# Optimization experiments

Measured on AMD Instinct MI355X. Metric: run time of the kernel, lower is better.

## Reference

```python
import math
import jax, jax.numpy as jnp
import numpy as np

K_KDE = 50
K_RIPS = 16
SCALE = 30.0
DESTNUM = 10
THRESHOLD = 1.0  # hardcoded in topograd_loss
N, D = 8192, 64


def _knn(x, k):
    """Brute-force k-NN with squared L2 distances (faiss IndexFlatL2 semantics,
    self included as nearest neighbour). Returns (sq_dists[N,k], idxs[N,k]),
    neighbours sorted by increasing distance."""
    sq = jnp.sum(x * x, axis=1)
    d = sq[:, None] + sq[None, :] - 2.0 * (x @ x.T)  # [N,N]
    neg, idx = jax.lax.top_k(-d, k)
    return -neg, idx


def _cluster(density, rips_idxs, threshold):
    """Union-find re-implementation of the numba `cluster` routine.
    Iterates points from high density (index N-1) to low; each point joins the
    entry of its highest-index upward neighbour; other upward neighbours'
    entries are merged if their persistence is below threshold, and every
    cross-entry comparison emits a persistence pair (entry_idx, ref_idx).
    Returns the raw pers_pairs array (without the [-1,-1] sentinel rows)."""
    n = density.shape[0]
    parent = np.arange(n)
    name = np.arange(n)  # name[root] = entry id (a point index)

    def find(i):
        root = i
        while parent[root] != root:
            root = parent[root]
        while parent[i] != root:  # path compression
            parent[i], i = root, parent[i]
        return root

    pairs = []
    for i in range(n - 2, -1, -1):
        nbr = rips_idxs[i]
        us = nbr[nbr > i]  # upward (denser, already-processed) neighbours
        if us.size == 0:
            continue  # point i forms its own singleton entry
        e_up = name[find(int(us.max()))]
        parent[find(i)] = find(e_up)  # append i to entry e_up
        for j in us:
            ei = name[find(int(j))]
            if ei != e_up:
                pairs.append((ei, i))
                if density[ei] - density[i] < threshold:
                    parent[find(ei)] = find(e_up)  # merge entry ei into e_up
    return np.asarray(pairs, dtype=np.int64).reshape(-1, 2)


def _pd_pairs(pairs, n):
    """For each unique entry id in pairs[:,0], keep (entry_id, max ref idx)."""
    maxref = np.full(n, -1, dtype=np.int64)
    np.maximum.at(maxref, pairs[:, 0], pairs[:, 1])
    uniq = np.unique(pairs[:, 0])
    return np.stack([uniq, maxref[uniq]], axis=1)


def setup_inputs() -> dict:
    key = jax.random.key(0)
    x = jax.random.normal(key, (N, D), dtype=jnp.float32)
    return {"x": x}


def reference(x):
    # --- KNN kernel density estimate (differentiable) ---
    vals, _ = _knn(x, K_KDE)
    res = jnp.sum(jnp.exp(-vals / SCALE), axis=1) / (K_KDE * SCALE)
    dens = res / jnp.max(res)
    # --- sort by ascending density ---
    sorted_idxs = jnp.argsort(dens)
    dens_s = dens[sorted_idxs]
    x_s = x[sorted_idxs]
    # --- delta-Rips graph on sorted points ---
    _, rips_idxs = _knn(x_s, K_RIPS)
    # --- persistence clustering (non-differentiable, host) ---
    pairs = _cluster(np.asarray(dens_s), np.asarray(rips_idxs), THRESHOLD)
    pd = jnp.asarray(_pd_pairs(pairs, x.shape[0]))  # [P,2] int64
    # --- topological loss ---
    oripd = dens_s[pd]  # [P,2] (birth, death) densities
    sidx = jnp.argsort(oripd[:, 0] - oripd[:, 1])  # ascending persistence
    changepairs = pd[sidx[:-DESTNUM]]
    nochangepairs = pd[sidx[-DESTNUM:-1]]
    dest = jax.lax.stop_gradient(oripd[sidx[-1]])  # torch.as_tensor detaches
    pd11 = dens_s[changepairs]
    weakdist = jnp.sum(pd11[:, 0] - pd11[:, 1]) / math.sqrt(2.0)
    strongdist = jnp.sum(jnp.linalg.norm(dens_s[nochangepairs] - dest, axis=1))
    return weakdist + strongdist
```

## Files before the change

### kernel.cpp

```cpp
#include <hip/hip_runtime.h>
#include <stdint.h>

#define NN 8192
#define DD 64

using bf16x8 = __attribute__((ext_vector_type(8))) short;
using f32x4  = __attribute__((ext_vector_type(4))) float;

__device__ __forceinline__ unsigned short f2bf(float f){
  unsigned u = __float_as_uint(f);
  return (unsigned short)((u + 0x7FFFu + ((u >> 16) & 1u)) >> 16);
}

__global__ __launch_bounds__(256) void k_pre(const float* __restrict__ x, float* __restrict__ xT,
                                             float* __restrict__ sq, int do_tr,
                                             uint4* __restrict__ xfrag, int do_frag){
  __shared__ float tile[64*65];
  const int tid = threadIdx.x;
  const int b = blockIdx.x;
  for (int k = 0; k < 4; ++k){
    const int idx4 = tid + k*256;
    const float4 v = ((const float4*)(x + (size_t)b*4096))[idx4];
    const int row = idx4 >> 4, d0 = (idx4 & 15) * 4;
    tile[row*65 + d0 + 0] = v.x;
    tile[row*65 + d0 + 1] = v.y;
    tile[row*65 + d0 + 2] = v.z;
    tile[row*65 + d0 + 3] = v.w;
  }
  __syncthreads();
  if (do_tr){
    const int jj = tid & 15;
    const int dq = tid >> 4;
    for (int k = 0; k < 4; ++k){
      const int d = dq + 16*k;
      float4 o;
      o.x = tile[(jj*4+0)*65 + d];
      o.y = tile[(jj*4+1)*65 + d];
      o.z = tile[(jj*4+2)*65 + d];
      o.w = tile[(jj*4+3)*65 + d];
      ((float4*)xT)[(size_t)d*2048 + b*16 + jj] = o;
    }
  }
  if (do_frag){
    for (int ch = tid; ch < 512; ch += 256){
      const int c  = ch & 15;
      const int q  = (ch >> 4) & 3;
      const int m  = (ch >> 6) & 1;
      const int gl = ch >> 7;
      const float* sp = tile + (gl*16 + c)*65 + m*32 + q*8;
      unsigned short h[8];
#pragma unroll
      for (int i2 = 0; i2 < 8; ++i2) h[i2] = f2bf(sp[i2]);
      uint4 o;
      o.x = (unsigned)h[0] | ((unsigned)h[1] << 16);
      o.y = (unsigned)h[2] | ((unsigned)h[3] << 16);
      o.z = (unsigned)h[4] | ((unsigned)h[5] << 16);
      o.w = (unsigned)h[6] | ((unsigned)h[7] << 16);
      xfrag[(size_t)b*512 + ch] = o;
    }
  }
  if (tid < 64){
    float acc = 0.f;
    const float* rp = tile + tid*65;
    for (int d = 0; d < 64; ++d) acc = fmaf(rp[d], rp[d], acc);
    sq[b*64 + tid] = acc;
  }
}

template<bool XT>
__device__ __forceinline__ void dists_1024(const float* __restrict__ x, const float* __restrict__ xT,
                                           const float* __restrict__ xi, int jbase, int tid,
                                           float acc[8][4]){
#pragma unroll
  for (int r = 0; r < 8; ++r)
#pragma unroll
    for (int q = 0; q < 4; ++q) acc[r][q] = 0.f;
  const int j0 = jbase + tid*4;
  for (int dq = 0; dq < 16; ++dq){
    float4 vj[4];
    if (XT){
#pragma unroll
      for (int s = 0; s < 4; ++s)
        vj[s] = ((const float4*)xT)[(size_t)(dq*4+s)*2048 + (j0 >> 2)];
    } else {
#pragma unroll
      for (int s = 0; s < 4; ++s){
        const int d = dq*4 + s;
        vj[s].x = x[(size_t)(j0+0)*64 + d];
        vj[s].y = x[(size_t)(j0+1)*64 + d];
        vj[s].z = x[(size_t)(j0+2)*64 + d];
        vj[s].w = x[(size_t)(j0+3)*64 + d];
      }
    }
#pragma unroll
    for (int r = 0; r < 8; ++r){
      const float4 wv = ((const float4*)(xi + r*64))[dq];
      acc[r][0] = fmaf(vj[0].x, wv.x, acc[r][0]);
      acc[r][1] = fmaf(vj[0].y, wv.x, acc[r][1]);
      acc[r][2] = fmaf(vj[0].z, wv.x, acc[r][2]);
      acc[r][3] = fmaf(vj[0].w, wv.x, acc[r][3]);
      acc[r][0] = fmaf(vj[1].x, wv.y, acc[r][0]);
      acc[r][1] = fmaf(vj[1].y, wv.y, acc[r][1]);
      acc[r][2] = fmaf(vj[1].z, wv.y, acc[r][2]);
      acc[r][3] = fmaf(vj[1].w, wv.y, acc[r][3]);
      acc[r][0] = fmaf(vj[2].x, wv.z, acc[r][0]);
      acc[r][1] = fmaf(vj[2].y, wv.z, acc[r][1]);
      acc[r][2] = fmaf(vj[2].z, wv.z, acc[r][2]);
      acc[r][3] = fmaf(vj[2].w, wv.z, acc[r][3]);
      acc[r][0] = fmaf(vj[3].x, wv.w, acc[r][0]);
      acc[r][1] = fmaf(vj[3].y, wv.w, acc[r][1]);
      acc[r][2] = fmaf(vj[3].z, wv.w, acc[r][2]);
      acc[r][3] = fmaf(vj[3].w, wv.w, acc[r][3]);
    }
  }
}

template<bool XT, bool MF>
__global__ __launch_bounds__(256) void k_cand(const float* __restrict__ x, const float* __restrict__ xT,
                                              const float* __restrict__ sq,
                                              float* __restrict__ res, unsigned short* __restrict__ nn16,
                                              const uint4* __restrict__ xfrag){
  __shared__ __align__(16) float xi[8*64];
  __shared__ float sqi_s[16];
  __shared__ float tubs[16];
  __shared__ __align__(16) unsigned long long cand[8*512];
  __shared__ unsigned ccnt[8];
  __shared__ unsigned ccnt2[8];
  __shared__ unsigned short candidx[MF ? 8*1024 : 16];
  float* samp = (float*)cand;
  const int tid = threadIdx.x;
  const int i0 = blockIdx.x * 8;
  for (int t = tid; t < 8*64; t += 256) xi[t] = x[(size_t)i0*64 + t];
  if (tid < 16){
    sqi_s[tid] = (tid < 8) ? sq[i0+tid] : 0.f;
    tubs[tid] = 0.f;
    if (tid < 8){ ccnt[tid] = 0u; ccnt2[tid] = 0u; }
  }
  __syncthreads();
  float sqir[8];
#pragma unroll
  for (int r = 0; r < 8; ++r) sqir[r] = sqi_s[r];

  const int w0 = (blockIdx.x * 1024) & 8191;
  {
    float acc[8][4];
    dists_1024<XT>(x, xT, xi, w0, tid, acc);
    float sqj[4];
#pragma unroll
    for (int q = 0; q < 4; ++q) sqj[q] = sq[w0 + tid*4 + q];
#pragma unroll
    for (int r = 0; r < 8; ++r)
#pragma unroll
      for (int q = 0; q < 4; ++q)
        samp[r*1024 + tid*4 + q] = (sqir[r] + sqj[q]) - 2.f*acc[r][q];
  }
  __syncthreads();
  {
    const int wv = tid >> 6, lane = tid & 63;
    for (int rr = 0; rr < 2; ++rr){
      const int r = wv + rr*4;
      float v[16];
#pragma unroll
      for (int k2 = 0; k2 < 16; ++k2) v[k2] = samp[r*1024 + lane + 64*k2];
      unsigned lo = 0u, hi = 0x7F800001u;
      while (hi - lo > 1u){
        const unsigned mid = (lo + hi) >> 1;
        const float pf = __uint_as_float(mid);
        int c = 0;
#pragma unroll
        for (int k2 = 0; k2 < 16; ++k2) c += (v[k2] < pf) ? 1 : 0;
#pragma unroll
        for (int off = 32; off; off >>= 1) c += __shfl_xor(c, off);
        if (c >= 32) hi = mid; else lo = mid;
      }
      if (lane == 0) tubs[r] = __uint_as_float(hi);
    }
  }
  __syncthreads();
  float tubr[8];
#pragma unroll
  for (int r = 0; r < 8; ++r) tubr[r] = tubs[r];
  for (int t = tid; t < 8*512; t += 256) cand[t] = ~0ULL;
  __syncthreads();

  if constexpr (MF){
    const int l   = tid & 63;
    const int w   = tid >> 6;
    const int qh  = l >> 4;
    const int c16 = l & 15;
    bf16x8 a0, a1;
#pragma unroll
    for (int i2 = 0; i2 < 8; ++i2){ a0[i2] = 0; a1[i2] = 0; }
    if (c16 < 8){
      const float* ap = xi + c16*64 + qh*8;
#pragma unroll
      for (int i2 = 0; i2 < 8; ++i2){
        a0[i2] = (short)f2bf(ap[i2]);
        a1[i2] = (short)f2bf(ap[i2 + 32]);
      }
    }
    float thr2v[4];
#pragma unroll
    for (int rg = 0; rg < 4; ++rg) thr2v[rg] = tubs[qh*4 + rg] + 2.0f - sqi_s[qh*4 + rg];

    const bf16x8* bfp = (const bf16x8*)xfrag + (size_t)w*128 + l;
    const float*  sqp = sq + w*16 + c16;
    for (int it = 0; it < 128; ++it){
      const bf16x8 b0 = bfp[(size_t)it*512];
      const bf16x8 b1 = bfp[(size_t)it*512 + 64];
      f32x4 acc = {0.f, 0.f, 0.f, 0.f};
      acc = __builtin_amdgcn_mfma_f32_16x16x32_bf16(a0, b0, acc, 0, 0, 0);
      acc = __builtin_amdgcn_mfma_f32_16x16x32_bf16(a1, b1, acc, 0, 0, 0);
      const float sqj = sqp[it*64];
      if (l < 32){
        const int j = (it*4 + w)*16 + c16;
#pragma unroll
        for (int rg = 0; rg < 4; ++rg){
          const float v = fmaf(-2.f, acc[rg], sqj);
          if (v < thr2v[rg]){
            const int r = qh*4 + rg;
            const unsigned pos = atomicAdd(&ccnt2[r], 1u);
            if (pos < 1024u) candidx[r*1024 + pos] = (unsigned short)j;
          }
        }
      }
    }
    __syncthreads();
    for (int r = 0; r < 8; ++r){
      const int cnt = ((int)ccnt2[r] < 1024) ? (int)ccnt2[r] : 1024;
      for (int t = tid; t < cnt; t += 256){
        const int j = candidx[r*1024 + t];
        const float* xj = x + (size_t)j*64;
        const float* xr = xi + r*64;
        float acc = 0.f;
#pragma unroll
        for (int d4 = 0; d4 < 16; ++d4){
          const float4 vj4 = ((const float4*)xj)[d4];
          const float4 wi4 = ((const float4*)xr)[d4];
          acc = fmaf(vj4.x, wi4.x, acc);
          acc = fmaf(vj4.y, wi4.y, acc);
          acc = fmaf(vj4.z, wi4.z, acc);
          acc = fmaf(vj4.w, wi4.w, acc);
        }
        const float dist = (sqir[r] + sq[j]) - 2.f*acc;
        if (dist < tubs[r]){
          const unsigned pos = atomicAdd(&ccnt[r], 1u);
          if (pos < 512u){
            unsigned u = __float_as_uint(dist);
            u = ((int)u < 0) ? ~u : (u | 0x80000000u);
            cand[r*512 + pos] = (((unsigned long long)u) << 13) | (unsigned)j;
          }
        }
      }
    }
  } else {
    for (int pass = 0; pass < 8; ++pass){
      const int jb = pass*1024;
      float acc[8][4];
      dists_1024<XT>(x, xT, xi, jb, tid, acc);
      const int j0 = jb + tid*4;
      float sqj[4];
#pragma unroll
      for (int q = 0; q < 4; ++q) sqj[q] = sq[j0 + q];
#pragma unroll
      for (int r = 0; r < 8; ++r){
#pragma unroll
        for (int q = 0; q < 4; ++q){
          const float dist = (sqir[r] + sqj[q]) - 2.f*acc[r][q];
          if (dist < tubr[r]){
            const unsigned pos = atomicAdd(&ccnt[r], 1u);
            if (pos < 512u){
              unsigned u = __float_as_uint(dist);
              u = ((int)u < 0) ? ~u : (u | 0x80000000u);
              cand[r*512 + pos] = (((unsigned long long)u) << 13) | (unsigned)(j0 + q);
            }
          }
        }
      }
    }
  }
  __syncthreads();

  for (int k = 2; k <= 512; k <<= 1){
    for (int jj2 = k >> 1; jj2 > 0; jj2 >>= 1){
      const int mm = tid;
      const int i = ((mm & ~(jj2-1)) << 1) | (mm & (jj2-1));
      const int p = i | jj2;
      const bool up2 = ((i & k) == 0);
#pragma unroll
      for (int r = 0; r < 8; ++r){
        unsigned long long a = cand[r*512+i], bb = cand[r*512+p];
        if ((a > bb) == up2){ cand[r*512+i] = bb; cand[r*512+p] = a; }
      }
      __syncthreads();
    }
  }

  const int wv2 = tid >> 6, lane2 = tid & 63;
  for (int rr = 0; rr < 2; ++rr){
    const int r = wv2*2 + rr;
    const unsigned long long kk = cand[r*512 + lane2];
    float e = 0.f;
    if (lane2 < 50){
      unsigned u2 = (unsigned)(kk >> 13);
      u2 = (u2 & 0x80000000u) ? (u2 & 0x7FFFFFFFu) : ~u2;
      e = expf(-__uint_as_float(u2) / 30.f);
    }
#pragma unroll
    for (int off = 32; off; off >>= 1) e += __shfl_down(e, off);
    if (lane2 == 0) res[i0+r] = e / 1500.f;
    if (lane2 < 16) nn16[(size_t)(i0+r)*16 + lane2] = (unsigned short)(kk & 8191ULL);
  }
}

__device__ __forceinline__ unsigned long long shfl64_xor(unsigned long long v, int off){
  return (((unsigned long long)(unsigned)__shfl_xor((int)(v >> 32), off)) << 32)
       | (unsigned long long)(unsigned)__shfl_xor((int)(v & 0xFFFFFFFFu), off);
}

__global__ __launch_bounds__(256) void k_rank(const float* __restrict__ res,
                                              unsigned short* __restrict__ rank,
                                              float* __restrict__ dens_s){
  __shared__ __align__(16) unsigned long long keys[NN];
  __shared__ float red[256];
  __shared__ unsigned short pcnt[256];
  const int tid = threadIdx.x;
  float m = 0.f;
  for (int t = tid; t < NN; t += 256) m = fmaxf(m, res[t]);
  red[tid] = m; __syncthreads();
  for (int o = 128; o; o >>= 1){ if (tid < o) red[tid] = fmaxf(red[tid], red[tid+o]); __syncthreads(); }
  const float mr = red[0];
  __syncthreads();
  for (int t = tid; t < NN; t += 256){
    const float dnv = res[t] / mr;
    keys[t] = (((unsigned long long)__float_as_uint(dnv)) << 13) | (unsigned)t;
  }
  __syncthreads();
  const int i = blockIdx.x*128 + (tid & 127);
  const unsigned long long ki = keys[i];
  const int j0 = (tid >> 7) * (NN/2);
  int c = 0;
#pragma unroll 8
  for (int j = 0; j < NN/2; ++j) c += (keys[j0 + j] < ki) ? 1 : 0;
  pcnt[tid] = (unsigned short)c;
  __syncthreads();
  if (tid < 128){
    const int r = (int)pcnt[tid] + (int)pcnt[tid + 128];
    rank[i] = (unsigned short)r;
    dens_s[r] = __uint_as_float((unsigned)(ki >> 13));
  }
}

__global__ __launch_bounds__(256) void k_ups(const unsigned short* __restrict__ rank,
                                             const unsigned short* __restrict__ nn16,
                                             unsigned short* __restrict__ ups_t){
  __shared__ __align__(16) unsigned short rk[NN];
  const int tid = threadIdx.x;
  for (int t = tid; t < NN/8; t += 256) ((uint4*)rk)[t] = ((const uint4*)rank)[t];
  __syncthreads();
  const int o = blockIdx.x*256 + tid;
  const int p = rk[o];
  const uint4 n0 = ((const uint4*)nn16)[(size_t)o*2];
  const uint4 n1 = ((const uint4*)nn16)[(size_t)o*2 + 1];
  unsigned nw[8] = {n0.x, n0.y, n0.z, n0.w, n1.x, n1.y, n1.z, n1.w};
  unsigned short outv[16];
  int cnt = 0;
  for (int k = 0; k < 16; ++k){
    const unsigned nb = (nw[k >> 1] >> ((k & 1) * 16)) & 0xFFFFu;
    const unsigned r = rk[nb];
    if ((int)r > p){
      int q = cnt++;
      while (q > 0 && outv[q-1] < (unsigned short)r){ outv[q] = outv[q-1]; --q; }
      outv[q] = (unsigned short)r;
    }
  }
  for (int k = cnt; k < 16; ++k) outv[k] = 0;
  unsigned short* dst = ups_t + (size_t)p*16;
  uint4 a, b;
  a.x = (unsigned)outv[0] | ((unsigned)outv[1] << 16);
  a.y = (unsigned)outv[2] | ((unsigned)outv[3] << 16);
  a.z = (unsigned)outv[4] | ((unsigned)outv[5] << 16);
  a.w = (unsigned)outv[6] | ((unsigned)outv[7] << 16);
  b.x = (unsigned)outv[8] | ((unsigned)outv[9] << 16);
  b.y = (unsigned)outv[10] | ((unsigned)outv[11] << 16);
  b.z = (unsigned)outv[12] | ((unsigned)outv[13] << 16);
  b.w = (unsigned)outv[14] | ((unsigned)outv[15] << 16);
  ((uint4*)dst)[0] = a;
  ((uint4*)dst)[1] = b;
}

__device__ __forceinline__ unsigned uf_find2(volatile unsigned short* comp, unsigned x){
  unsigned r = comp[x];
  while (true){
    const unsigned g = comp[r];
    if (g == r) break;
    comp[x] = (unsigned short)g;
    x = r; r = g;
  }
  return r;
}

__global__ __launch_bounds__(1024) void k_msf(const float* __restrict__ dens_s,
                                              unsigned short* __restrict__ ups_t,
                                              unsigned long long* __restrict__ edges,
                                              int edgecap,
                                              float* __restrict__ out){
  __shared__ __align__(16) float dens[NN];
  __shared__ __align__(16) unsigned short P[NN];
  __shared__ __align__(16) unsigned short pkid[NN];
  __shared__ __align__(16) unsigned short death[NN];
  __shared__ __align__(16) unsigned short pkrank[4096];
  __shared__ __align__(16) unsigned short comp[4096];
  __shared__ __align__(16) unsigned short hook[4096];
  __shared__ __align__(16) unsigned bestv[4096];
  __shared__ __align__(16) unsigned long long msf[4096];
  __shared__ unsigned long long wred[17];
  __shared__ unsigned long long sel[10];
  __shared__ unsigned ecnt_s, ecnt2_s, mcnt_s, chg_s, flat_s, dcnt_s;
  unsigned* scan1 = (unsigned*)msf;
  float* red = (float*)msf;
  unsigned* dlist = bestv;

  const int tid = threadIdx.x;
  const int lane = tid & 63;

  for (int t = tid; t < NN/4; t += 1024)
    ((float4*)dens)[t] = ((const float4*)dens_s)[t];
  for (int t = tid; t < NN; t += 1024){
    const unsigned u0 = ups_t[(size_t)t*16];
    P[t] = (u0 == 0u) ? (unsigned short)t : (unsigned short)u0;
    death[t] = 0xFFFFu;
  }
  if (tid == 0){ ecnt_s = 0u; mcnt_s = 0u; dcnt_s = 0u; }
  __syncthreads();

  for (int rd = 0; rd < 13; ++rd){
    for (int pp = 0; pp < 8; ++pp){
      const int p = tid + pp*1024;
      const unsigned v = P[p];
      const unsigned w2 = P[v];
      if (w2 != v) P[p] = (unsigned short)w2;
    }
    __syncthreads();
  }

  {
    const int p0 = tid*8;
    int c = 0;
    for (int k = 0; k < 8; ++k) c += (P[p0+k] == (unsigned short)(p0+k)) ? 1 : 0;
    scan1[tid] = (unsigned)c; __syncthreads();
    for (int s = 1; s < 1024; s <<= 1){
      const unsigned v = scan1[tid];
      const unsigned u = (tid >= s) ? scan1[tid-s] : 0u;
      __syncthreads();
      scan1[tid] = v + u;
      __syncthreads();
    }
    int base = (int)scan1[tid] - c;
    for (int k = 0; k < 8; ++k){
      const int p = p0 + k;
      if (P[p] == (unsigned short)p){
        pkid[p] = (unsigned short)base;
        if (base < 4096) pkrank[base] = (unsigned short)p;
        ++base;
      }
    }
  }
  __syncthreads();
  int Npk = (int)scan1[1023];
  if (Npk > 4096) Npk = 4096;
  __syncthreads();

  for (int pp = 0; pp < 8; ++pp){
    const int p = tid + pp*1024;
    const uint4 a4 = ((const uint4*)ups_t)[(size_t)p*2];
    const uint4 b4 = ((const uint4*)ups_t)[(size_t)p*2 + 1];
    unsigned uu[8] = {a4.x, a4.y, a4.z, a4.w, b4.x, b4.y, b4.z, b4.w};
    unsigned edv[15];
    int nd = 0;
    const unsigned u0 = uu[0] & 0xFFFFu;
    if (u0 != 0u){
      const unsigned m0 = P[u0];
      const unsigned m0id = pkid[m0];
      for (int k = 1; k < 16; ++k){
        const unsigned uk = (uu[k >> 1] >> ((k & 1) * 16)) & 0xFFFFu;
        if (uk == 0u) break;
        const unsigned v = P[uk];
        if (v == m0) continue;
        const unsigned vid = pkid[v];
        bool dup = false;
        for (int j = 0; j < nd; ++j) dup = dup || ((edv[j] >> 16) == vid);
        if (dup) continue;
        edv[nd++] = (vid << 16) | m0id;
      }
    }
    unsigned off = (unsigned)nd;
    for (int s = 1; s < 64; s <<= 1){
      const unsigned o = (unsigned)__shfl_up((int)off, s);
      if (lane >= s) off += o;
    }
    const unsigned tot = (unsigned)__shfl((int)off, 63);
    unsigned wb = 0u;
    if (lane == 0 && tot) wb = atomicAdd(&ecnt_s, tot);
    wb = (unsigned)__shfl((int)wb, 0);
    const unsigned mybase = wb + off - (unsigned)nd;
    for (int k = 0; k < nd; ++k){
      const unsigned pos = mybase + (unsigned)k;
      if ((int)pos < edgecap)
        edges[pos] = (((unsigned long long)(unsigned)p) << 32) | (unsigned long long)edv[k];
    }
  }
  __syncthreads();
  int Ecur = ((int)ecnt_s < edgecap) ? (int)ecnt_s : edgecap;

  unsigned long long* eb_in  = edges;
  unsigned long long* eb_out = (unsigned long long*)ups_t;
  for (int t = tid; t < Npk; t += 1024) comp[t] = (unsigned short)t;
  __syncthreads();
  for (int round = 0; round < 16 && Ecur > 0; ++round){
    for (int t = tid; t < Npk; t += 1024){ bestv[t] = 0u; hook[t] = 0xFFFFu; }
    if (tid == 0){ chg_s = 0u; ecnt2_s = 0u; }
    __syncthreads();
    for (int base = 0; base < Ecur; base += 1024){
      const int e = base + tid;
      bool keep = false;
      unsigned long long ed = 0ULL;
      if (e < Ecur){
        ed = eb_in[e];
        const unsigned a = (unsigned)(ed >> 16) & 0xFFFFu;
        const unsigned b = (unsigned)ed & 0xFFFFu;
        const unsigned ra = comp[a], rb = comp[b];
        if (ra != rb){
          keep = true;
          const unsigned key = ((((unsigned)(ed >> 32)) + 1u) << 18) | (unsigned)e;
          atomicMax(&bestv[ra], key);
          atomicMax(&bestv[rb], key);
        }
      }
      const unsigned long long bal = __ballot(keep);
      const unsigned cnt = (unsigned)__popcll(bal);
      const unsigned pfx = (unsigned)__popcll(bal & ((1ULL << lane) - 1ULL));
      unsigned wb = 0u;
      if (lane == 0 && cnt) wb = atomicAdd(&ecnt2_s, cnt);
      wb = (unsigned)__shfl((int)wb, 0);
      if (keep && (wb + pfx) < 32768u) eb_out[wb + pfx] = ed;
    }
    __syncthreads();
    for (int t = tid; t < Npk; t += 1024){
      if (comp[t] == (unsigned short)t && bestv[t] != 0u){
        const unsigned long long ed = eb_in[bestv[t] & 0x3FFFFu];
        const unsigned a = (unsigned)(ed >> 16) & 0xFFFFu;
        const unsigned b = (unsigned)ed & 0xFFFFu;
        const unsigned ra = comp[a], rb = comp[b];
        hook[t] = (unsigned short)((ra == (unsigned)t) ? rb : ra);
      }
    }
    __syncthreads();
    for (int t = tid; t < Npk; t += 1024){
      const unsigned o = hook[t];
      if (o != 0xFFFFu && !(hook[o] == (unsigned short)t && (unsigned)t < o)){
        comp[t] = (unsigned short)o;
        chg_s = 1u;
        const unsigned long long ed = eb_in[bestv[t] & 0x3FFFFu];
        const unsigned pos = atomicAdd(&mcnt_s, 1u);
        if (pos < 4096u) msf[pos] = (((ed >> 32) + 1ULL) << 32) | (ed & 0xFFFFFFFFULL);
      }
    }
    __syncthreads();
    for (;;){
      if (tid == 0) flat_s = 0u;
      __syncthreads();
      for (int t = tid; t < Npk; t += 1024){
        const unsigned c = comp[t];
        const unsigned cc = comp[c];
        if (cc != c){ comp[t] = (unsigned short)cc; flat_s = 1u; }
      }
      __syncthreads();
      if (flat_s == 0u) break;
    }
    const int En = ((int)ecnt2_s < 32768) ? (int)ecnt2_s : 32767;
    const unsigned ch = chg_s;
    __syncthreads();
    Ecur = En;
    { unsigned long long* t2 = eb_in; eb_in = eb_out; eb_out = t2; }
    if (ch == 0u) break;
  }

  const int M = ((int)mcnt_s < 4096) ? (int)mcnt_s : 4095;
  int W = 64; while (W < M) W <<= 1;
  for (int t = M + tid; t < W; t += 1024) msf[t] = 0ULL;
  for (int t = tid; t < Npk; t += 1024) comp[t] = (unsigned short)t;
  __syncthreads();
  for (int k = 2; k <= W; k <<= 1){
    for (int j = k >> 1; j > 0; j >>= 1){
      for (int m2 = tid; m2 < W/2; m2 += 1024){
        const int i = ((m2 & ~(j-1)) << 1) | (m2 & (j-1));
        const int p = i | j;
        const bool up = ((i & k) == 0);
        const unsigned long long a = msf[i], b = msf[p];
        if ((a < b) == up){ msf[i] = b; msf[p] = a; }
      }
      __syncthreads();
    }
  }

  {
    const int nb = (M + 63) >> 6;
    for (int bch = 0; bch < nb; ++bch){
      if (tid < 64){
        const int ei = bch*64 + lane;
        unsigned ra = 0xFFFFu, rb = 0xFFFFu, wgt = 0u;
        if (ei < M){
          const unsigned long long e = msf[ei];
          const unsigned a = ((unsigned)e >> 16) & 0xFFFFu;
          const unsigned b = (unsigned)e & 0xFFFFu;
          wgt = (unsigned)(e >> 32) - 1u;
          ra = uf_find2(comp, a);
          rb = uf_find2(comp, b);
        }
        unsigned kra = 0xFFFFu, krb = 0xFFFFu;
        for (int i = 0; i < 64; ++i){
          const unsigned rai = (unsigned)__builtin_amdgcn_readlane((int)ra, i);
          const unsigned rbi = (unsigned)__builtin_amdgcn_readlane((int)rb, i);
          if (rai == 0xFFFFu || rai == rbi) continue;
          if (lane == i){ kra = rai; krb = rbi; }
          ra = (ra == rai) ? rbi : ra;
          rb = (rb == rai) ? rbi : rb;
        }
        if (kra != 0xFFFFu){
          death[pkrank[kra]] = (unsigned short)wgt;
          comp[kra] = (unsigned short)krb;
        }
      }
      __syncthreads();
      for (int t = tid; t < Npk; t += 1024){
        const unsigned c = comp[t];
        const unsigned cc = comp[c];
        if (cc != c) comp[t] = (unsigned short)cc;
      }
      __syncthreads();
    }
  }
  __syncthreads();

  float s = 0.f;
  for (int e = tid; e < NN; e += 1024){
    const int dr = death[e];
    if (dr != 0xFFFF) s += dens[e] - dens[dr];
  }
  red[tid] = s; __syncthreads();
  for (int o = 512; o; o >>= 1){ if (tid < o) red[tid] += red[tid+o]; __syncthreads(); }
  const float S = red[0];

  for (int e8 = 0; e8 < 8; ++e8){
    const int e = tid + e8*1024;
    const int dr = death[e];
    const bool have = (dr != 0xFFFF);
    const unsigned long long bal = __ballot(have);
    const unsigned cnt = (unsigned)__popcll(bal);
    const unsigned pfx = (unsigned)__popcll(bal & ((1ULL << lane) - 1ULL));
    unsigned wb = 0u;
    if (lane == 0 && cnt) wb = atomicAdd(&dcnt_s, cnt);
    wb = (unsigned)__shfl((int)wb, 0);
    if (have && (wb + pfx) < 4096u) dlist[wb + pfx] = ((unsigned)e << 13) | (unsigned)dr;
  }
  __syncthreads();
  const int Dm = ((int)dcnt_s < 4096) ? (int)dcnt_s : 4096;

  unsigned long long last = ~0ULL;
  for (int t10 = 0; t10 < 10; ++t10){
    unsigned long long km = 0ULL;
    for (int i = tid; i < Dm; i += 1024){
      const unsigned pk = dlist[i];
      const unsigned e = pk >> 13, dr = pk & 8191u;
      const float pers = dens[e] - dens[dr];
      const unsigned long long k = (((unsigned long long)__float_as_uint(pers)) << 13) | e;
      if (k < last && k > km) km = k;
    }
    for (int off = 32; off; off >>= 1){
      const unsigned long long o = shfl64_xor(km, off);
      km = (o > km) ? o : km;
    }
    if (lane == 0) wred[tid >> 6] = km;
    __syncthreads();
    if (tid < 64){
      unsigned long long v = (tid < 16) ? wred[tid] : 0ULL;
      for (int off = 8; off; off >>= 1){
        const unsigned long long o = shfl64_xor(v, off);
        v = (o > v) ? o : v;
      }
      if (tid == 0) wred[16] = v;
    }
    __syncthreads();
    const unsigned long long st = wred[16];
    if (tid == 0) sel[t10] = st;
    last = st;
    __syncthreads();
  }
  if (tid == 0){
    float top = 0.f;
    for (int t10 = 0; t10 < 10; ++t10)
      if (sel[t10]) top += __uint_as_float((unsigned)(sel[t10] >> 13));
    float strong = 0.f, dest0 = 0.f, dest1 = 0.f;
    if (sel[0]){
      const unsigned e0 = (unsigned)(sel[0] & 8191ULL);
      dest0 = dens[e0]; dest1 = dens[death[e0]];
    }
    for (int t10 = 1; t10 < 10; ++t10){
      if (!sel[t10]) continue;
      const unsigned e = (unsigned)(sel[t10] & 8191ULL);
      const float a = dens[e] - dest0;
      const float b = dens[death[e]] - dest1;
      strong += sqrtf(a*a + b*b);
    }
    out[0] = (S - top) / 1.41421356237309515f + strong;
  }
}

extern "C" void kernel_launch(void* const* d_in, const int* in_sizes, int n_in,
                              void* d_out, int out_size, void* d_ws, size_t ws_size,
                              hipStream_t stream){
  const float* x = (const float*)d_in[0];
  char* w = (char*)d_ws;
  float*          sq     = (float*)(w + 0);
  float*          res    = (float*)(w + 32768);
  float*          dens_s = (float*)(w + 65536);
  unsigned short* rank   = (unsigned short*)(w + 98304);
  unsigned short* nn16   = (unsigned short*)(w + 114688);
  unsigned short* ups_t  = (unsigned short*)(w + 376832);
  float*          xT     = (float*)(w + 655360);
  uint4*          xfrag  = (uint4*)(w + 655360 + (size_t)NN*DD*4);
  const int use_xt = (ws_size >= (size_t)(655360 + NN*DD*4)) ? 1 : 0;
  const int use_mf = (ws_size >= (size_t)(655360 + NN*DD*4 + NN*DD*2)) ? 1 : 0;
  unsigned long long* edges = use_xt ? (unsigned long long*)(w + 655360)
                                     : (unsigned long long*)(w + 114688);
  const int edgecap = use_xt ? 262143 : 32767;

  k_pre<<<128, 256, 0, stream>>>(x, xT, sq, use_xt, xfrag, use_mf);
  if (use_mf)      k_cand<true , true ><<<1024, 256, 0, stream>>>(x, xT, sq, res, nn16, xfrag);
  else if (use_xt) k_cand<true , false><<<1024, 256, 0, stream>>>(x, xT, sq, res, nn16, xfrag);
  else             k_cand<false, false><<<1024, 256, 0, stream>>>(x, xT, sq, res, nn16, xfrag);
  k_rank<<<64, 256, 0, stream>>>(res, rank, dens_s);
  k_ups <<<32, 256, 0, stream>>>(rank, nn16, ups_t);
  k_msf <<<1, 1024, 0, stream>>>(dens_s, ups_t, edges, edgecap, (float*)d_out);
}
```

Measured before the change: 633.3 us.

## Replace atomic candidate lists with ballot bitmasks and prefetch MFMA fragments

In the MFMA filtering pass, threshold hits are no longer appended to a per-row LDS list through shared-memory atomics. Each wave now builds hit bitmasks with __ballot and stores them in LDS, and the exact refinement pass walks those bitmasks with ctz. The B-fragment and squared-norm loads are also software-prefetched four iterations ahead in registers, to hide global latency behind the MFMAs. This removes atomic contention and the 1024-candidate cap. The cost is more register pressure, and the refinement work is spread unevenly across threads, since each one scans a 16-bit mask.

```diff
diff --git a/kernel.cpp b/kernel.cpp
--- a/kernel.cpp
+++ b/kernel.cpp
@@ -125,8 +125,7 @@
   __shared__ float tubs[16];
   __shared__ __align__(16) unsigned long long cand[8*512];
   __shared__ unsigned ccnt[8];
-  __shared__ unsigned ccnt2[8];
-  __shared__ unsigned short candidx[MF ? 8*1024 : 16];
+  __shared__ __align__(16) unsigned bm32s[MF ? 512*4 : 4];
   float* samp = (float*)cand;
   const int tid = threadIdx.x;
   const int i0 = blockIdx.x * 8;
@@ -134,7 +133,7 @@
   if (tid < 16){
     sqi_s[tid] = (tid < 8) ? sq[i0+tid] : 0.f;
     tubs[tid] = 0.f;
-    if (tid < 8){ ccnt[tid] = 0u; ccnt2[tid] = 0u; }
+    if (tid < 8) ccnt[tid] = 0u;
   }
   __syncthreads();
   float sqir[8];
@@ -199,39 +198,65 @@
         a1[i2] = (short)f2bf(ap[i2 + 32]);
       }
     }
-    float thr2v[4];
-#pragma unroll
-    for (int rg = 0; rg < 4; ++rg) thr2v[rg] = tubs[qh*4 + rg] + 2.0f - sqi_s[qh*4 + rg];
+    const float thr2v0 = tubs[qh*4+0] + 2.0f - sqi_s[qh*4+0];
+    const float thr2v1 = tubs[qh*4+1] + 2.0f - sqi_s[qh*4+1];
+    const float thr2v2 = tubs[qh*4+2] + 2.0f - sqi_s[qh*4+2];
+    const float thr2v3 = tubs[qh*4+3] + 2.0f - sqi_s[qh*4+3];
 
     const bf16x8* bfp = (const bf16x8*)xfrag + (size_t)w*128 + l;
     const float*  sqp = sq + w*16 + c16;
-    for (int it = 0; it < 128; ++it){
-      const bf16x8 b0 = bfp[(size_t)it*512];
-      const bf16x8 b1 = bfp[(size_t)it*512 + 64];
+
+    auto fbody = [&](bf16x8 B0v, bf16x8 B1v, float SJ, int ITV){
       f32x4 acc = {0.f, 0.f, 0.f, 0.f};
-      acc = __builtin_amdgcn_mfma_f32_16x16x32_bf16(a0, b0, acc, 0, 0, 0);
-      acc = __builtin_amdgcn_mfma_f32_16x16x32_bf16(a1, b1, acc, 0, 0, 0);
-      const float sqj = sqp[it*64];
-      if (l < 32){
-        const int j = (it*4 + w)*16 + c16;
-#pragma unroll
-        for (int rg = 0; rg < 4; ++rg){
-          const float v = fmaf(-2.f, acc[rg], sqj);
-          if (v < thr2v[rg]){
-            const int r = qh*4 + rg;
-            const unsigned pos = atomicAdd(&ccnt2[r], 1u);
-            if (pos < 1024u) candidx[r*1024 + pos] = (unsigned short)j;
-          }
-        }
-      }
-    }
-    __syncthreads();
-    for (int r = 0; r < 8; ++r){
-      const int cnt = ((int)ccnt2[r] < 1024) ? (int)ccnt2[r] : 1024;
-      for (int t = tid; t < cnt; t += 256){
-        const int j = candidx[r*1024 + t];
+      acc = __builtin_amdgcn_mfma_f32_16x16x32_bf16(a0, B0v, acc, 0, 0, 0);
+      acc = __builtin_amdgcn_mfma_f32_16x16x32_bf16(a1, B1v, acc, 0, 0, 0);
+      const float v0 = fmaf(-2.f, acc[0], SJ);
+      const float v1 = fmaf(-2.f, acc[1], SJ);
+      const float v2 = fmaf(-2.f, acc[2], SJ);
+      const float v3 = fmaf(-2.f, acc[3], SJ);
+      const unsigned long long m0 = __ballot(v0 < thr2v0);
+      const unsigned long long m1 = __ballot(v1 < thr2v1);
+      const unsigned long long m2 = __ballot(v2 < thr2v2);
+      const unsigned long long m3 = __ballot(v3 < thr2v3);
+      const int cc = ITV*4 + w;
+      if (l == 0){
+        bm32s[cc*4+0] = ((unsigned)m0 & 0xFFFFu) | (((unsigned)m1 & 0xFFFFu) << 16);
+        bm32s[cc*4+1] = ((unsigned)m2 & 0xFFFFu) | (((unsigned)m3 & 0xFFFFu) << 16);
+      } else if (l == 16){
+        bm32s[cc*4+2] = (((unsigned)m0 >> 16) & 0xFFFFu) | ((((unsigned)m1 >> 16) & 0xFFFFu) << 16);
+        bm32s[cc*4+3] = (((unsigned)m2 >> 16) & 0xFFFFu) | ((((unsigned)m3 >> 16) & 0xFFFFu) << 16);
+      }
+    };
+
+    bf16x8 pA0 = bfp[0],    pA1 = bfp[64];
+    bf16x8 pB0 = bfp[512],  pB1 = bfp[512+64];
+    bf16x8 pC0 = bfp[1024], pC1 = bfp[1024+64];
+    bf16x8 pD0 = bfp[1536], pD1 = bfp[1536+64];
+    float sA = sqp[0], sB = sqp[64], sC = sqp[128], sD = sqp[192];
+    for (int itb = 0; itb < 128; itb += 4){
+      fbody(pA0, pA1, sA, itb);
+      if (itb + 4 < 128){ pA0 = bfp[(size_t)(itb+4)*512]; pA1 = bfp[(size_t)(itb+4)*512+64]; sA = sqp[(itb+4)*64]; }
+      fbody(pB0, pB1, sB, itb+1);
+      if (itb + 5 < 128){ pB0 = bfp[(size_t)(itb+5)*512]; pB1 = bfp[(size_t)(itb+5)*512+64]; sB = sqp[(itb+5)*64]; }
+      fbody(pC0, pC1, sC, itb+2);
+      if (itb + 6 < 128){ pC0 = bfp[(size_t)(itb+6)*512]; pC1 = bfp[(size_t)(itb+6)*512+64]; sC = sqp[(itb+6)*64]; }
+      fbody(pD0, pD1, sD, itb+3);
+      if (itb + 7 < 128){ pD0 = bfp[(size_t)(itb+7)*512]; pD1 = bfp[(size_t)(itb+7)*512+64]; sD = sqp[(itb+7)*64]; }
+    }
+    __syncthreads();
+
+    const unsigned short* bmu = (const unsigned short*)bm32s;
+    for (int idx = tid; idx < 4096; idx += 256){
+      const int cc = idx >> 3, r = idx & 7;
+      unsigned msk = (unsigned)bmu[cc*8 + r];
+      const float* xr = xi + r*64;
+      const float sqi_r = sqir[r];
+      const float tub_r = tubr[r];
+      while (msk){
+        const int bpos = __builtin_ctz(msk);
+        msk &= msk - 1u;
+        const int j = cc*16 + bpos;
         const float* xj = x + (size_t)j*64;
-        const float* xr = xi + r*64;
         float acc = 0.f;
 #pragma unroll
         for (int d4 = 0; d4 < 16; ++d4){
@@ -242,8 +267,8 @@
           acc = fmaf(vj4.z, wi4.z, acc);
           acc = fmaf(vj4.w, wi4.w, acc);
         }
-        const float dist = (sqir[r] + sq[j]) - 2.f*acc;
-        if (dist < tubs[r]){
+        const float dist = (sqi_r + sq[j]) - 2.f*acc;
+        if (dist < tub_r){
           const unsigned pos = atomicAdd(&ccnt[r], 1u);
           if (pos < 512u){
             unsigned u = __float_as_uint(dist);
```

New measurement: 641.9 us. No clear change (+1.4%).

## Split fused candidate kernel into sample, MFMA filter bitmask, and exact-sort kernels

Applied to the files above, without the earlier changes.

The single k_cand kernel is split into three kernels. k_samp computes the per-row sample threshold. k_filt runs the bf16 MFMA prefilter with software-prefetched fragments and writes a per-pair bitmask to global memory. k_csort decodes the bitmask, recomputes exact distances and bitonic-sorts. The split lowers per-kernel shared-memory and register pressure and removes LDS atomics from the MFMA loop, which should allow higher occupancy. In exchange it adds two extra launches and an 8 MB global bitmask round-trip, and it needs a larger workspace or it falls back to the old path.

```diff
diff --git a/kernel.cpp b/kernel.cpp
--- a/kernel.cpp
+++ b/kernel.cpp
@@ -115,123 +115,155 @@
   }
 }
 
-template<bool XT, bool MF>
-__global__ __launch_bounds__(256) void k_cand(const float* __restrict__ x, const float* __restrict__ xT,
-                                              const float* __restrict__ sq,
-                                              float* __restrict__ res, unsigned short* __restrict__ nn16,
-                                              const uint4* __restrict__ xfrag){
+template<bool XT>
+__global__ __launch_bounds__(256) void k_samp(const float* __restrict__ x, const float* __restrict__ xT,
+                                              const float* __restrict__ sq, float* __restrict__ tub){
   __shared__ __align__(16) float xi[8*64];
-  __shared__ float sqi_s[16];
-  __shared__ float tubs[16];
-  __shared__ __align__(16) unsigned long long cand[8*512];
-  __shared__ unsigned ccnt[8];
-  __shared__ unsigned ccnt2[8];
-  __shared__ unsigned short candidx[MF ? 8*1024 : 16];
-  float* samp = (float*)cand;
+  __shared__ float sqi_s[8];
+  __shared__ __align__(16) float samp[8*1024];
   const int tid = threadIdx.x;
   const int i0 = blockIdx.x * 8;
   for (int t = tid; t < 8*64; t += 256) xi[t] = x[(size_t)i0*64 + t];
-  if (tid < 16){
-    sqi_s[tid] = (tid < 8) ? sq[i0+tid] : 0.f;
-    tubs[tid] = 0.f;
-    if (tid < 8){ ccnt[tid] = 0u; ccnt2[tid] = 0u; }
-  }
+  if (tid < 8) sqi_s[tid] = sq[i0+tid];
   __syncthreads();
   float sqir[8];
 #pragma unroll
   for (int r = 0; r < 8; ++r) sqir[r] = sqi_s[r];
 
   const int w0 = (blockIdx.x * 1024) & 8191;
-  {
-    float acc[8][4];
-    dists_1024<XT>(x, xT, xi, w0, tid, acc);
-    float sqj[4];
-#pragma unroll
-    for (int q = 0; q < 4; ++q) sqj[q] = sq[w0 + tid*4 + q];
-#pragma unroll
-    for (int r = 0; r < 8; ++r)
-#pragma unroll
-      for (int q = 0; q < 4; ++q)
-        samp[r*1024 + tid*4 + q] = (sqir[r] + sqj[q]) - 2.f*acc[r][q];
-  }
-  __syncthreads();
-  {
-    const int wv = tid >> 6, lane = tid & 63;
-    for (int rr = 0; rr < 2; ++rr){
-      const int r = wv + rr*4;
-      float v[16];
-#pragma unroll
-      for (int k2 = 0; k2 < 16; ++k2) v[k2] = samp[r*1024 + lane + 64*k2];
-      unsigned lo = 0u, hi = 0x7F800001u;
-      while (hi - lo > 1u){
-        const unsigned mid = (lo + hi) >> 1;
-        const float pf = __uint_as_float(mid);
-        int c = 0;
-#pragma unroll
-        for (int k2 = 0; k2 < 16; ++k2) c += (v[k2] < pf) ? 1 : 0;
-#pragma unroll
-        for (int off = 32; off; off >>= 1) c += __shfl_xor(c, off);
-        if (c >= 32) hi = mid; else lo = mid;
-      }
-      if (lane == 0) tubs[r] = __uint_as_float(hi);
-    }
-  }
-  __syncthreads();
-  float tubr[8];
-#pragma unroll
-  for (int r = 0; r < 8; ++r) tubr[r] = tubs[r];
+  float acc[8][4];
+  dists_1024<XT>(x, xT, xi, w0, tid, acc);
+  float sqj[4];
+#pragma unroll
+  for (int q = 0; q < 4; ++q) sqj[q] = sq[w0 + tid*4 + q];
+#pragma unroll
+  for (int r = 0; r < 8; ++r)
+#pragma unroll
+    for (int q = 0; q < 4; ++q)
+      samp[r*1024 + tid*4 + q] = (sqir[r] + sqj[q]) - 2.f*acc[r][q];
+  __syncthreads();
+  const int wv = tid >> 6, lane = tid & 63;
+  for (int rr = 0; rr < 2; ++rr){
+    const int r = wv + rr*4;
+    float v[16];
+#pragma unroll
+    for (int k2 = 0; k2 < 16; ++k2) v[k2] = samp[r*1024 + lane + 64*k2];
+    unsigned lo = 0u, hi = 0x7F800001u;
+    while (hi - lo > 1u){
+      const unsigned mid = (lo + hi) >> 1;
+      const float pf = __uint_as_float(mid);
+      int c = 0;
+#pragma unroll
+      for (int k2 = 0; k2 < 16; ++k2) c += (v[k2] < pf) ? 1 : 0;
+#pragma unroll
+      for (int off = 32; off; off >>= 1) c += __shfl_xor(c, off);
+      if (c >= 32) hi = mid; else lo = mid;
+    }
+    if (lane == 0) tub[i0 + r] = __uint_as_float(hi);
+  }
+}
+
+__global__ __launch_bounds__(256) void k_filt(const float* __restrict__ x, const float* __restrict__ sq,
+                                              const float* __restrict__ tub,
+                                              const uint4* __restrict__ xfrag,
+                                              unsigned char* __restrict__ nib){
+  const int tid = threadIdx.x;
+  const int l   = tid & 63;
+  const int w   = tid >> 6;
+  const int qh  = l >> 4;
+  const int c16 = l & 15;
+  const int i0  = blockIdx.x * 8;
+
+  bf16x8 a0, a1;
+#pragma unroll
+  for (int i2 = 0; i2 < 8; ++i2){ a0[i2] = 0; a1[i2] = 0; }
+  if (c16 < 8){
+    const float* ap = x + (size_t)(i0 + c16)*64 + qh*8;
+#pragma unroll
+    for (int i2 = 0; i2 < 8; ++i2){
+      a0[i2] = (short)f2bf(ap[i2]);
+      a1[i2] = (short)f2bf(ap[i2 + 32]);
+    }
+  }
+  float thr2[4];
+#pragma unroll
+  for (int rg = 0; rg < 4; ++rg){
+    int row = qh*4 + rg; row = (row < 8) ? row : 0;
+    thr2[rg] = tub[i0 + row] + 2.0f - sq[i0 + row];
+  }
+
+  const bf16x8* bfp = (const bf16x8*)xfrag + (size_t)w*128 + l;
+  const float*  sqp = sq + w*16 + c16;
+  unsigned char* nb = nib + (size_t)blockIdx.x*8192 + w*16 + c16;
+
+  bf16x8 A0 = bfp[0],   A1 = bfp[64];     float SA = sqp[0];
+  bf16x8 B0 = bfp[512], B1 = bfp[512+64]; float SB = sqp[64];
+  for (int it = 0; it < 128; it += 2){
+    const int n2 = (it+2 < 128) ? it+2 : 126;
+    const int n3 = (it+3 < 128) ? it+3 : 127;
+    bf16x8 N0 = bfp[(size_t)n2*512], N1 = bfp[(size_t)n2*512 + 64];
+    bf16x8 M0 = bfp[(size_t)n3*512], M1 = bfp[(size_t)n3*512 + 64];
+    const float SN = sqp[n2*64], SM = sqp[n3*64];
+    {
+      f32x4 acc = {0.f, 0.f, 0.f, 0.f};
+      acc = __builtin_amdgcn_mfma_f32_16x16x32_bf16(a0, A0, acc, 0, 0, 0);
+      acc = __builtin_amdgcn_mfma_f32_16x16x32_bf16(a1, A1, acc, 0, 0, 0);
+      unsigned m4 = 0u;
+      m4 |= (fmaf(-2.f, acc[0], SA) < thr2[0]) ? 1u : 0u;
+      m4 |= (fmaf(-2.f, acc[1], SA) < thr2[1]) ? 2u : 0u;
+      m4 |= (fmaf(-2.f, acc[2], SA) < thr2[2]) ? 4u : 0u;
+      m4 |= (fmaf(-2.f, acc[3], SA) < thr2[3]) ? 8u : 0u;
+      const unsigned pm = (unsigned)__shfl((int)m4, (l + 16) & 63);
+      if (l < 16) nb[it*64] = (unsigned char)(m4 | (pm << 4));
+    }
+    {
+      f32x4 acc = {0.f, 0.f, 0.f, 0.f};
+      acc = __builtin_amdgcn_mfma_f32_16x16x32_bf16(a0, B0, acc, 0, 0, 0);
+      acc = __builtin_amdgcn_mfma_f32_16x16x32_bf16(a1, B1, acc, 0, 0, 0);
+      unsigned m4 = 0u;
+      m4 |= (fmaf(-2.f, acc[0], SB) < thr2[0]) ? 1u : 0u;
+      m4 |= (fmaf(-2.f, acc[1], SB) < thr2[1]) ? 2u : 0u;
+      m4 |= (fmaf(-2.f, acc[2], SB) < thr2[2]) ? 4u : 0u;
+      m4 |= (fmaf(-2.f, acc[3], SB) < thr2[3]) ? 8u : 0u;
+      const unsigned pm = (unsigned)__shfl((int)m4, (l + 16) & 63);
+      if (l < 16) nb[(it+1)*64] = (unsigned char)(m4 | (pm << 4));
+    }
+    A0 = N0; A1 = N1; SA = SN;
+    B0 = M0; B1 = M1; SB = SM;
+  }
+}
+
+__global__ __launch_bounds__(256) void k_csort(const float* __restrict__ x, const float* __restrict__ sq,
+                                               const float* __restrict__ tub,
+                                               const unsigned char* __restrict__ nib,
+                                               float* __restrict__ res, unsigned short* __restrict__ nn16){
+  __shared__ __align__(16) float xi[8*68];
+  __shared__ float sqi_s[8];
+  __shared__ float tubs[8];
+  __shared__ __align__(16) unsigned long long cand[8*512];
+  __shared__ unsigned ccnt[8];
+  const int tid = threadIdx.x;
+  const int i0 = blockIdx.x * 8;
+  for (int t = tid; t < 8*64; t += 256) xi[(t >> 6)*68 + (t & 63)] = x[(size_t)i0*64 + t];
+  if (tid < 8){ sqi_s[tid] = sq[i0+tid]; tubs[tid] = tub[i0+tid]; ccnt[tid] = 0u; }
   for (int t = tid; t < 8*512; t += 256) cand[t] = ~0ULL;
   __syncthreads();
 
-  if constexpr (MF){
-    const int l   = tid & 63;
-    const int w   = tid >> 6;
-    const int qh  = l >> 4;
-    const int c16 = l & 15;
-    bf16x8 a0, a1;
-#pragma unroll
-    for (int i2 = 0; i2 < 8; ++i2){ a0[i2] = 0; a1[i2] = 0; }
-    if (c16 < 8){
-      const float* ap = xi + c16*64 + qh*8;
-#pragma unroll
-      for (int i2 = 0; i2 < 8; ++i2){
-        a0[i2] = (short)f2bf(ap[i2]);
-        a1[i2] = (short)f2bf(ap[i2 + 32]);
-      }
-    }
-    float thr2v[4];
-#pragma unroll
-    for (int rg = 0; rg < 4; ++rg) thr2v[rg] = tubs[qh*4 + rg] + 2.0f - sqi_s[qh*4 + rg];
-
-    const bf16x8* bfp = (const bf16x8*)xfrag + (size_t)w*128 + l;
-    const float*  sqp = sq + w*16 + c16;
-    for (int it = 0; it < 128; ++it){
-      const bf16x8 b0 = bfp[(size_t)it*512];
-      const bf16x8 b1 = bfp[(size_t)it*512 + 64];
-      f32x4 acc = {0.f, 0.f, 0.f, 0.f};
-      acc = __builtin_amdgcn_mfma_f32_16x16x32_bf16(a0, b0, acc, 0, 0, 0);
-      acc = __builtin_amdgcn_mfma_f32_16x16x32_bf16(a1, b1, acc, 0, 0, 0);
-      const float sqj = sqp[it*64];
-      if (l < 32){
-        const int j = (it*4 + w)*16 + c16;
-#pragma unroll
-        for (int rg = 0; rg < 4; ++rg){
-          const float v = fmaf(-2.f, acc[rg], sqj);
-          if (v < thr2v[rg]){
-            const int r = qh*4 + rg;
-            const unsigned pos = atomicAdd(&ccnt2[r], 1u);
-            if (pos < 1024u) candidx[r*1024 + pos] = (unsigned short)j;
-          }
-        }
-      }
-    }
-    __syncthreads();
-    for (int r = 0; r < 8; ++r){
-      const int cnt = ((int)ccnt2[r] < 1024) ? (int)ccnt2[r] : 1024;
-      for (int t = tid; t < cnt; t += 256){
-        const int j = candidx[r*1024 + t];
+  const uint4* nb4 = (const uint4*)(nib + (size_t)blockIdx.x*8192);
+  for (int u = tid; u < 512; u += 256){
+    const uint4 v4 = nb4[u];
+    unsigned wds[4] = {v4.x, v4.y, v4.z, v4.w};
+#pragma unroll
+    for (int ww = 0; ww < 4; ++ww){
+      unsigned wvv = wds[ww];
+      while (wvv){
+        const int bit = __builtin_ctz(wvv);
+        wvv &= wvv - 1u;
+        const int byte = bit >> 3;
+        const int r = bit & 7;
+        const int j = u*16 + ww*4 + byte;
         const float* xj = x + (size_t)j*64;
-        const float* xr = xi + r*64;
+        const float* xr = xi + r*68;
         float acc = 0.f;
 #pragma unroll
         for (int d4 = 0; d4 < 16; ++d4){
@@ -242,38 +274,132 @@
           acc = fmaf(vj4.z, wi4.z, acc);
           acc = fmaf(vj4.w, wi4.w, acc);
         }
-        const float dist = (sqir[r] + sq[j]) - 2.f*acc;
+        const float dist = (sqi_s[r] + sq[j]) - 2.f*acc;
         if (dist < tubs[r]){
+          const unsigned pos = atomicAdd(&ccnt[r], 1u);
+          if (pos < 512u){
+            unsigned u2 = __float_as_uint(dist);
+            u2 = ((int)u2 < 0) ? ~u2 : (u2 | 0x80000000u);
+            cand[r*512 + pos] = (((unsigned long long)u2) << 13) | (unsigned)j;
+          }
+        }
+      }
+    }
+  }
+  __syncthreads();
+
+  for (int k = 2; k <= 512; k <<= 1){
+    for (int jj2 = k >> 1; jj2 > 0; jj2 >>= 1){
+      const int mm = tid;
+      const int i = ((mm & ~(jj2-1)) << 1) | (mm & (jj2-1));
+      const int p = i | jj2;
+      const bool up2 = ((i & k) == 0);
+#pragma unroll
+      for (int r = 0; r < 8; ++r){
+        unsigned long long a = cand[r*512+i], bb = cand[r*512+p];
+        if ((a > bb) == up2){ cand[r*512+i] = bb; cand[r*512+p] = a; }
+      }
+      __syncthreads();
+    }
+  }
+
+  const int wv2 = tid >> 6, lane2 = tid & 63;
+  for (int rr = 0; rr < 2; ++rr){
+    const int r = wv2*2 + rr;
+    const unsigned long long kk = cand[r*512 + lane2];
+    float e = 0.f;
+    if (lane2 < 50){
+      unsigned u2 = (unsigned)(kk >> 13);
+      u2 = (u2 & 0x80000000u) ? (u2 & 0x7FFFFFFFu) : ~u2;
+      e = expf(-__uint_as_float(u2) / 30.f);
+    }
+#pragma unroll
+    for (int off = 32; off; off >>= 1) e += __shfl_down(e, off);
+    if (lane2 == 0) res[i0+r] = e / 1500.f;
+    if (lane2 < 16) nn16[(size_t)(i0+r)*16 + lane2] = (unsigned short)(kk & 8191ULL);
+  }
+}
+
+template<bool XT>
+__global__ __launch_bounds__(256) void k_cand(const float* __restrict__ x, const float* __restrict__ xT,
+                                              const float* __restrict__ sq,
+                                              float* __restrict__ res, unsigned short* __restrict__ nn16){
+  __shared__ float xi[8*64];
+  __shared__ float sqi_s[8];
+  __shared__ float tubs[8];
+  __shared__ __align__(16) unsigned long long cand[8*512];
+  __shared__ unsigned ccnt[8];
+  float* samp = (float*)cand;
+  const int tid = threadIdx.x;
+  const int i0 = blockIdx.x * 8;
+  for (int t = tid; t < 8*64; t += 256) xi[t] = x[(size_t)i0*64 + t];
+  if (tid < 8){ sqi_s[tid] = sq[i0+tid]; ccnt[tid] = 0u; }
+  __syncthreads();
+  float sqir[8];
+#pragma unroll
+  for (int r = 0; r < 8; ++r) sqir[r] = sqi_s[r];
+
+  const int w0 = (blockIdx.x * 1024) & 8191;
+  {
+    float acc[8][4];
+    dists_1024<XT>(x, xT, xi, w0, tid, acc);
+    float sqj[4];
+#pragma unroll
+    for (int q = 0; q < 4; ++q) sqj[q] = sq[w0 + tid*4 + q];
+#pragma unroll
+    for (int r = 0; r < 8; ++r)
+#pragma unroll
+      for (int q = 0; q < 4; ++q)
+        samp[r*1024 + tid*4 + q] = (sqir[r] + sqj[q]) - 2.f*acc[r][q];
+  }
+  __syncthreads();
+  {
+    const int wv = tid >> 6, lane = tid & 63;
+    for (int rr = 0; rr < 2; ++rr){
+      const int r = wv + rr*4;
+      float v[16];
+#pragma unroll
+      for (int k2 = 0; k2 < 16; ++k2) v[k2] = samp[r*1024 + lane + 64*k2];
+      unsigned lo = 0u, hi = 0x7F800001u;
+      while (hi - lo > 1u){
+        const unsigned mid = (lo + hi) >> 1;
+        const float pf = __uint_as_float(mid);
+        int c = 0;
+#pragma unroll
+        for (int k2 = 0; k2 < 16; ++k2) c += (v[k2] < pf) ? 1 : 0;
+#pragma unroll
+        for (int off = 32; off; off >>= 1) c += __shfl_xor(c, off);
+        if (c >= 32) hi = mid; else lo = mid;
+      }
+      if (lane == 0) tubs[r] = __uint_as_float(hi);
+    }
+  }
+  __syncthreads();
+  float tubr[8];
+#pragma unroll
+  for (int r = 0; r < 8; ++r) tubr[r] = tubs[r];
+  for (int t = tid; t < 8*512; t += 256) cand[t] = ~0ULL;
+  __syncthreads();
+
+  for (int pass = 0; pass < 8; ++pass){
+    const int jb = pass*1024;
+    float acc[8][4];
+    dists_1024<XT>(x, xT, xi, jb, tid, acc);
+    const int j0 = jb + tid*4;
+    float sqj[4];
+#pragma unroll
+    for (int q = 0; q < 4; ++q) sqj[q] = sq[j0 + q];
+#pragma unroll
+    for (int r = 0; r < 8; ++r){
+#pragma unroll
+      for (int q = 0; q < 4; ++q){
+        const float dist = (sqir[r] + sqj[q]) - 2.f*acc[r][q];
+        if (dist < tubr[r]){
           const unsigned pos = atomicAdd(&ccnt[r], 1u);
           if (pos < 512u){
             unsigned u = __float_as_uint(dist);
             u = ((int)u < 0) ? ~u : (u | 0x80000000u);
-            cand[r*512 + pos] = (((unsigned long long)u) << 13) | (unsigned)j;
-          }
-        }
-      }
-    }
-  } else {
-    for (int pass = 0; pass < 8; ++pass){
-      const int jb = pass*1024;
-      float acc[8][4];
-      dists_1024<XT>(x, xT, xi, jb, tid, acc);
-      const int j0 = jb + tid*4;
-      float sqj[4];
-#pragma unroll
-      for (int q = 0; q < 4; ++q) sqj[q] = sq[j0 + q];
-#pragma unroll
-      for (int r = 0; r < 8; ++r){
-#pragma unroll
-        for (int q = 0; q < 4; ++q){
-          const float dist = (sqir[r] + sqj[q]) - 2.f*acc[r][q];
-          if (dist < tubr[r]){
-            const unsigned pos = atomicAdd(&ccnt[r], 1u);
-            if (pos < 512u){
-              unsigned u = __float_as_uint(dist);
-              u = ((int)u < 0) ? ~u : (u | 0x80000000u);
-              cand[r*512 + pos] = (((unsigned long long)u) << 13) | (unsigned)(j0 + q);
-            }
+            cand[r*512 + pos] = (((unsigned long long)u) << 13) | (unsigned)(j0 + q);
           }
         }
       }
@@ -729,17 +855,25 @@
   unsigned short* nn16   = (unsigned short*)(w + 114688);
   unsigned short* ups_t  = (unsigned short*)(w + 376832);
   float*          xT     = (float*)(w + 655360);
-  uint4*          xfrag  = (uint4*)(w + 655360 + (size_t)NN*DD*4);
-  const int use_xt = (ws_size >= (size_t)(655360 + NN*DD*4)) ? 1 : 0;
-  const int use_mf = (ws_size >= (size_t)(655360 + NN*DD*4 + NN*DD*2)) ? 1 : 0;
+  uint4*          xfrag  = (uint4*)(w + 2752512);
+  float*          tub    = (float*)(w + 3801088);
+  unsigned char*  nib    = (unsigned char*)(w + 3833856);
+  const int use_xt  = (ws_size >= (size_t)2752512) ? 1 : 0;
+  const int use_mf2 = (ws_size >= (size_t)(3833856 + 8*1024*1024)) ? 1 : 0;
   unsigned long long* edges = use_xt ? (unsigned long long*)(w + 655360)
                                      : (unsigned long long*)(w + 114688);
   const int edgecap = use_xt ? 262143 : 32767;
 
-  k_pre<<<128, 256, 0, stream>>>(x, xT, sq, use_xt, xfrag, use_mf);
-  if (use_mf)      k_cand<true , true ><<<1024, 256, 0, stream>>>(x, xT, sq, res, nn16, xfrag);
-  else if (use_xt) k_cand<true , false><<<1024, 256, 0, stream>>>(x, xT, sq, res, nn16, xfrag);
-  else             k_cand<false, false><<<1024, 256, 0, stream>>>(x, xT, sq, res, nn16, xfrag);
+  k_pre<<<128, 256, 0, stream>>>(x, xT, sq, use_xt, xfrag, use_mf2);
+  if (use_mf2){
+    k_samp<true><<<1024, 256, 0, stream>>>(x, xT, sq, tub);
+    k_filt<<<1024, 256, 0, stream>>>(x, sq, tub, xfrag, nib);
+    k_csort<<<1024, 256, 0, stream>>>(x, sq, tub, nib, res, nn16);
+  } else if (use_xt){
+    k_cand<true ><<<1024, 256, 0, stream>>>(x, xT, sq, res, nn16);
+  } else {
+    k_cand<false><<<1024, 256, 0, stream>>>(x, xT, sq, res, nn16);
+  }
   k_rank<<<64, 256, 0, stream>>>(res, rank, dens_s);
   k_ups <<<32, 256, 0, stream>>>(rank, nn16, ups_t);
   k_msf <<<1, 1024, 0, stream>>>(dens_s, ups_t, edges, edgecap, (float*)d_out);
```

Measured after the change: 574.5 us. 1.1x faster.
